# Optimization experiments

Measured on AMD Instinct MI355X. Metric: run time of the kernel, lower is better.

## Reference

```python
import jax, jax.numpy as jnp
import numpy as np

HIDDEN = 512
HEADS = 8
HEAD_DIM = HIDDEN // HEADS
MAX_DIST = 10
B, N = 16, 512
EPS = 1e-5


def _layer_norm(x, g, b):
    mu = jnp.mean(x, axis=-1, keepdims=True)
    var = jnp.mean(jnp.square(x - mu), axis=-1, keepdims=True)
    return (x - mu) * jax.lax.rsqrt(var + EPS) * g + b


def setup_inputs() -> dict:
    key = jax.random.key(0)
    ks = jax.random.split(key, 16)
    s = 0.02
    inp = {
        "x": jax.random.normal(ks[0], (B, N, HIDDEN), jnp.float32),
        "distances": jax.random.randint(ks[1], (B, N, N), 0, MAX_DIST, jnp.int32),
        "edge_features": jax.random.normal(ks[2], (B, N, N), jnp.float32),
        "attn_mask": jax.random.randint(ks[3], (B, N), 0, 2).astype(bool),
        "Wq": jax.random.normal(ks[4], (HIDDEN, HIDDEN), jnp.float32) * s,
        "bq": jnp.zeros((HIDDEN,), jnp.float32),
        "Wk": jax.random.normal(ks[5], (HIDDEN, HIDDEN), jnp.float32) * s,
        "bk": jnp.zeros((HIDDEN,), jnp.float32),
        "Wv": jax.random.normal(ks[6], (HIDDEN, HIDDEN), jnp.float32) * s,
        "bv": jnp.zeros((HIDDEN,), jnp.float32),
        "Wo": jax.random.normal(ks[7], (HIDDEN, HIDDEN), jnp.float32) * s,
        "bo": jnp.zeros((HIDDEN,), jnp.float32),
        "spatial_emb": jax.random.normal(ks[8], (MAX_DIST, HEADS), jnp.float32) * s,
        "edge_w": jax.random.normal(ks[9], (HEADS,), jnp.float32) * s,
        "edge_b": jnp.zeros((HEADS,), jnp.float32),
        "ln1_g": jnp.ones((HIDDEN,), jnp.float32),
        "ln1_b": jnp.zeros((HIDDEN,), jnp.float32),
        "ln2_g": jnp.ones((HIDDEN,), jnp.float32),
        "ln2_b": jnp.zeros((HIDDEN,), jnp.float32),
        "W1": jax.random.normal(ks[10], (HIDDEN, 4 * HIDDEN), jnp.float32) * s,
        "b1": jnp.zeros((4 * HIDDEN,), jnp.float32),
        "W2": jax.random.normal(ks[11], (4 * HIDDEN, HIDDEN), jnp.float32) * s,
        "b2": jnp.zeros((HIDDEN,), jnp.float32),
    }
    return inp


def reference(x, distances, edge_features, attn_mask, Wq, bq, Wk, bk, Wv, bv,
              Wo, bo, spatial_emb, edge_w, edge_b, ln1_g, ln1_b, ln2_g, ln2_b,
              W1, b1, W2, b2):
    b, n, _ = x.shape
    q = (x @ Wq + bq).reshape(b, n, HEADS, HEAD_DIM)
    k = (x @ Wk + bk).reshape(b, n, HEADS, HEAD_DIM)
    v = (x @ Wv + bv).reshape(b, n, HEADS, HEAD_DIM)
    # [b, h, i, j] attention scores
    scores = jnp.einsum('bihd,bjhd->bhij', q, k) / np.sqrt(HEAD_DIM).astype(np.float32)
    spatial_bias = spatial_emb[distances]                       # [b, i, j, h]
    edge_bias = edge_features[..., None] * edge_w + edge_b      # [b, i, j, h]
    scores = scores + jnp.transpose(spatial_bias + edge_bias, (0, 3, 1, 2))
    scores = jnp.where(attn_mask[:, None, None, :], -jnp.inf, scores)
    attn = jax.nn.softmax(scores, axis=-1)
    out = jnp.einsum('bhij,bjhd->bihd', attn, v).reshape(b, n, HIDDEN)
    out = out @ Wo + bo
    h = _layer_norm(x + out, ln1_g, ln1_b)
    ffn = jax.nn.relu(h @ W1 + b1) @ W2 + b2
    return _layer_norm(h + ffn, ln2_g, ln2_b)
```

## Files before the change

kernel.cpp:

```cpp
#include <hip/hip_runtime.h>
#include <stdint.h>
#include <stddef.h>

#define SEQ   512
#define HID   512
#define NHEAD 8
#define HD    64
#define NBATCH 16
#define NTOK  8192
#define MAXD  10
#define LOG2E 1.4426950408889634f

typedef __attribute__((ext_vector_type(8))) short short8;
typedef __attribute__((ext_vector_type(4))) float f32x4;

typedef __attribute__((address_space(3))) void        as3_void;
typedef const __attribute__((address_space(1))) void  as1_cvoid;

#define MFMA16(a,b,c) __builtin_amdgcn_mfma_f32_16x16x32_bf16((a),(b),(c),0,0,0)

__device__ __forceinline__ float bf2f(uint16_t u){ return __uint_as_float(((uint32_t)u)<<16); }
__device__ __forceinline__ uint16_t f2bf(float f){
  uint32_t i = __float_as_uint(f);
  return (uint16_t)((i + 0x7fffu + ((i>>16)&1u)) >> 16);
}
__device__ __forceinline__ uint16_t f2bf_rtz(float f){
  return (uint16_t)(__float_as_uint(f) >> 16);
}

enum { EPI_BF16=0, EPI_F32=3, EPI_RELU=4 };

__global__ __launch_bounds__(256) void prep_kernel(
    const float* __restrict__ x, uint16_t* __restrict__ xb,
    const float* __restrict__ Wq, const float* __restrict__ Wk,
    const float* __restrict__ Wv, const float* __restrict__ Wo,
    const float* __restrict__ W1, const float* __restrict__ W2,
    uint16_t* __restrict__ tq, uint16_t* __restrict__ tk,
    uint16_t* __restrict__ tv, uint16_t* __restrict__ to_,
    uint16_t* __restrict__ t1, uint16_t* __restrict__ t2)
{
  int id = blockIdx.x;
  if (id >= 3072){
    int i = (id-3072)*256 + threadIdx.x;
    if (i < NTOK*HID/4){
      float4 v = *(const float4*)(x + (size_t)i*4);
      *(ushort4*)(xb + (size_t)i*4) =
          make_ushort4(f2bf(v.x), f2bf(v.y), f2bf(v.z), f2bf(v.w));
    }
    return;
  }
  __shared__ uint16_t tile[32][33];
  const float* in; uint16_t* out; int R, C, tx, ty;
  if (id < 1024) {
    int m = id >> 8, loc = id & 255;
    in  = (m==0)?Wq:(m==1)?Wk:(m==2)?Wv:Wo;
    out = (m==0)?tq:(m==1)?tk:(m==2)?tv:to_;
    R = 512; C = 512; ty = loc>>4; tx = loc&15;
  } else if (id < 2048) {
    int loc = id-1024; in=W1; out=t1; R=512; C=2048; ty=loc>>6; tx=loc&63;
  } else {
    int loc = id-2048; in=W2; out=t2; R=2048; C=512; ty=loc>>4; tx=loc&15;
  }
  int bx = tx*32, by = ty*32;
  int lx = threadIdx.x & 31, ly = threadIdx.x >> 5;
  #pragma unroll
  for (int i=ly; i<32; i+=8) tile[i][lx] = f2bf(in[(size_t)(by+i)*C + bx+lx]);
  __syncthreads();
  #pragma unroll
  for (int i=ly; i<32; i+=8) out[(size_t)(bx+i)*R + by+lx] = tile[lx][i];
}

__global__ __launch_bounds__(512) void pack_bias(
    const int*   __restrict__ dist,
    const float* __restrict__ edge,
    const int*   __restrict__ mask,
    uint32_t*    __restrict__ outp)
{
  __shared__ int   dl[16][260];
  __shared__ float el[16][260];
  __shared__ int   ml[512];
  const int b  = blockIdx.y;
  const int it = blockIdx.x;
  const int t  = threadIdx.x;
  ml[t] = mask[b*SEQ + t];

  #pragma unroll
  for (int jh=0; jh<2; ++jh){
    if (jh) __syncthreads();
    {
      const int r  = t >> 5;
      const int c0 = (t & 31) * 8;
      const size_t g = ((size_t)b*SEQ + it*16 + r)*SEQ + jh*256 + c0;
      *(int4*)&dl[r][c0]     = *(const int4*)&dist[g];
      *(int4*)&dl[r][c0+4]   = *(const int4*)&dist[g+4];
      *(float4*)&el[r][c0]   = *(const float4*)&edge[g];
      *(float4*)&el[r][c0+4] = *(const float4*)&edge[g+4];
    }
    __syncthreads();
    {
      const int i   = t & 15;
      const int j0p = (t >> 4) * 8;
      const int jt  = jh*4 + (j0p >> 6);
      const int jn  = (j0p >> 4) & 3;
      const int lg  = (j0p & 15) >> 2;
      uint32_t w[8];
      #pragma unroll
      for (int e=0; e<8; ++e){
        const int jl = j0p + e;
        const int jg = jh*256 + jl;
        const uint32_t d  = (uint32_t)dl[i][jl] & 0xFFu;
        const uint32_t mk = (ml[jg] ? 1u : 0u) << 8;
        w[e] = ((uint32_t)f2bf(el[i][jl]) << 16) | mk | d;
      }
      uint32_t* ob = outp + ((((size_t)b*32 + it)*8 + jt)*64)*16;
      const int lane0 = lg*16 + i, lane1 = (lg+1)*16 + i;
      *(uint4*)&ob[lane0*16 + jn*4] = make_uint4(w[0],w[1],w[2],w[3]);
      *(uint4*)&ob[lane1*16 + jn*4] = make_uint4(w[4],w[5],w[6],w[7]);
    }
  }
}

template<int BM, int BN>
__device__ __forceinline__ void gemm_tile_mainloop(
    const uint16_t* __restrict__ A, const uint16_t* __restrict__ Bt,
    int K, int m0, int n0, uint16_t* lA, uint16_t* lB,
    f32x4 acc[4][(BM==128)?4:((BN==128)?2:1)])
{
  constexpr int NJ  = (BM==128)?4:((BN==128)?2:1);
  constexpr int ARD = BM/32;
  constexpr int BRD = BN/32;
  const int t = threadIdx.x;
  const int w = t>>6, l = t&63;
  const int lg = l>>4, lc = l&15;
  const int wr = (BM==128)?(w>>1):0;
  const int wc = (BM==128)?(w&1):w;
  const int swz = lc & 7;
  const int kSteps = K>>6;

  auto stage = [&](int kt, int buf){
    const int k0 = kt<<6;
    #pragma unroll
    for (int rd=0; rd<ARD; ++rd){
      const int e   = rd*2048 + t*8;
      const int row = e>>6;
      const int col = (((e>>3)&7) ^ (row&7))*8;
      const uint16_t* ga = A + (size_t)(m0+row)*K + (k0+col);
      char* la = (char*)(lA + buf*(BM*64)) + rd*4096 + w*1024;
      __builtin_amdgcn_global_load_lds((as1_cvoid*)ga, (as3_void*)la, 16, 0, 0);
    }
    #pragma unroll
    for (int rd=0; rd<BRD; ++rd){
      const int e   = rd*2048 + t*8;
      const int row = e>>6;
      const int col = (((e>>3)&7) ^ (row&7))*8;
      const uint16_t* gb = Bt + (size_t)(n0+row)*K + (k0+col);
      char* lb = (char*)(lB + buf*(BN*64)) + rd*4096 + w*1024;
      __builtin_amdgcn_global_load_lds((as1_cvoid*)gb, (as3_void*)lb, 16, 0, 0);
    }
  };

  auto compute = [&](const uint16_t* rA, const uint16_t* rB){
    #pragma unroll
    for (int kk=0; kk<2; ++kk){
      const int cc = (kk*4 + lg) ^ swz;
      short8 af[4], bfr[NJ];
      #pragma unroll
      for (int i=0;i<4;i++)
        af[i]  = *(const short8*)&rA[(wr*64 + i*16 + lc)*64 + cc*8];
      #pragma unroll
      for (int j=0;j<NJ;j++)
        bfr[j] = *(const short8*)&rB[(wc*16*NJ + j*16 + lc)*64 + cc*8];
      #pragma unroll
      for (int i=0;i<4;i++)
        #pragma unroll
        for (int j=0;j<NJ;j++)
          acc[i][j] = MFMA16(af[i], bfr[j], acc[i][j]);
    }
  };

  stage(0, 0);
  __syncthreads();
  int cur = 0;
  for (int kt=0; kt<kSteps; ++kt){
    if (kt+1 < kSteps) stage(kt+1, cur^1);
    compute(lA + cur*(BM*64), lB + cur*(BN*64));
    __syncthreads();
    cur ^= 1;
  }
}

template<int EPI, int BM, int BN>
__global__ __launch_bounds__(256,2) void gemm_bt(
    const uint16_t* __restrict__ A, const uint16_t* __restrict__ Bt,
    const float* __restrict__ bias, void* __restrict__ outp,
    int M, int N, int K)
{
  constexpr int NJ = (BM==128)?4:((BN==128)?2:1);
  __shared__ uint16_t lA[2*BM*64];
  __shared__ uint16_t lB[2*BN*64];
  f32x4 acc[4][NJ];
  #pragma unroll
  for (int i=0;i<4;i++)
    #pragma unroll
    for (int j=0;j<NJ;j++){ f32x4 z = {0.f,0.f,0.f,0.f}; acc[i][j]=z; }
  const int m0 = blockIdx.x*BM, n0 = blockIdx.y*BN;
  gemm_tile_mainloop<BM,BN>(A, Bt, K, m0, n0, lA, lB, acc);

  const int t=threadIdx.x, w=t>>6, l=t&63, lg=l>>4, lc=l&15;
  const int wr=(BM==128)?(w>>1):0, wc=(BM==128)?(w&1):w;
  #pragma unroll
  for (int j=0;j<NJ;j++){
    const int col = n0 + wc*16*NJ + j*16 + lc;
    const float bs = bias[col];
    #pragma unroll
    for (int i=0;i<4;i++){
      const int rowb = m0 + wr*64 + i*16 + lg*4;
      #pragma unroll
      for (int r=0;r<4;r++){
        float v = acc[i][j][r] + bs;
        if constexpr (EPI==EPI_RELU)   v = fmaxf(v, 0.f);
        if constexpr (EPI==EPI_F32)
          ((float*)outp)[(size_t)(rowb+r)*N + col] = v;
        else
          ((uint16_t*)outp)[(size_t)(rowb+r)*N + col] = f2bf(v);
      }
    }
  }
}

__global__ __launch_bounds__(256,2) void qkv_gemm(
    const uint16_t* __restrict__ x,
    const uint16_t* __restrict__ wtq, const uint16_t* __restrict__ wtk,
    const uint16_t* __restrict__ wtv,
    const float* __restrict__ bq, const float* __restrict__ bk,
    const float* __restrict__ bv,
    uint16_t* __restrict__ qo, uint16_t* __restrict__ kp,
    uint16_t* __restrict__ vp)
{
  __shared__ uint16_t lA[2*128*64];
  __shared__ uint16_t lB[2*128*64];
  const int z = blockIdx.z;
  const uint16_t* Bt = (z==0)?wtq:(z==1)?wtk:wtv;
  const float*  bias = (z==0)?bq :(z==1)?bk :bv;
  f32x4 acc[4][4];
  #pragma unroll
  for (int i=0;i<4;i++)
    #pragma unroll
    for (int j=0;j<4;j++){ f32x4 zz = {0.f,0.f,0.f,0.f}; acc[i][j]=zz; }
  const int m0 = blockIdx.x*128, n0 = blockIdx.y*128;
  gemm_tile_mainloop<128,128>(x, Bt, HID, m0, n0, lA, lB, acc);

  const int t=threadIdx.x, w=t>>6, l=t&63, lg=l>>4, lc=l&15, wr=w>>1, wc=w&1;
  if (z==0){
    const float scale = 0.125f * LOG2E;
    #pragma unroll
    for (int j=0;j<4;j++){
      const int col = n0 + wc*64 + j*16 + lc;
      const float bs = bias[col];
      #pragma unroll
      for (int i=0;i<4;i++){
        const int rowb = m0 + wr*64 + i*16 + lg*4;
        #pragma unroll
        for (int r=0;r<4;r++)
          qo[(size_t)(rowb+r)*HID + col] = f2bf((acc[i][j][r] + bs)*scale);
      }
    }
  } else if (z==1){
    #pragma unroll
    for (int j=0;j<4;j++){
      const int col = n0 + wc*64 + j*16 + lc;
      const float bs = bias[col];
      const int h_ = col>>6, cm = col&63, kk = cm>>5, lgk = (cm>>3)&3, e = col&7;
      #pragma unroll
      for (int i=0;i<4;i++){
        const int rowb = m0 + wr*64 + i*16 + lg*4;
        #pragma unroll
        for (int r=0;r<4;r++){
          const int tok = rowb + r;
          const int b_ = tok>>9, tl = tok&511;
          const int jt = tl>>6, jn = (tl>>4)&3, lck = tl&15;
          kp[((((size_t)(b_*8+h_)*8 + jt)*4 + jn)*2 + kk)*512
             + (lgk*16 + lck)*8 + e] = f2bf(acc[i][j][r] + bs);
        }
      }
    }
  } else {
    #pragma unroll
    for (int j=0;j<4;j++){
      const int col = n0 + wc*64 + j*16 + lc;
      const float bs = bias[col];
      const int h_ = col>>6, dn = (col>>4)&3, lcv = col&15;
      #pragma unroll
      for (int i=0;i<4;i++){
        const int rowb = m0 + wr*64 + i*16 + lg*4;
        const int b_ = rowb>>9, tl = rowb&511;
        const int jt = tl>>6, kk = (tl>>5)&1, lgv = (tl>>3)&3, e0 = tl&7;
        *(ushort4*)&vp[((((size_t)(b_*8+h_)*8 + jt)*2 + kk)*4 + dn)*512
                       + (lgv*16 + lcv)*8 + e0] =
            make_ushort4(f2bf(acc[i][j][0]+bs), f2bf(acc[i][j][1]+bs),
                         f2bf(acc[i][j][2]+bs), f2bf(acc[i][j][3]+bs));
      }
    }
  }
}

__global__ __launch_bounds__(512,4) void attn_kernel(
    const uint16_t* __restrict__ q,
    const uint16_t* __restrict__ kp,
    const uint16_t* __restrict__ vp,
    const uint32_t* __restrict__ biasp,
    const float*    __restrict__ semb,
    const float*    __restrict__ ew,
    const float*    __restrict__ eb,
    uint16_t* __restrict__ out)
{
  __shared__ float sp_rep[NHEAD][64][11];
  __shared__ uint16_t plds[NHEAD][2][16*64];
  const int b  = blockIdx.y;
  const int it = blockIdx.x;
  const int i0 = it*16;
  const int t  = threadIdx.x;
  const int h  = t>>6, l = t&63, lg = l>>4, lc = l&15;
  for (int i = t; i < NHEAD*64*MAXD; i += 512){
    const int hh = i / (64*MAXD), rem = i % (64*MAXD);
    const int a = rem / MAXD, d = rem % MAXD;
    sp_rep[hh][a][d] = (semb[d*NHEAD + hh] + eb[hh]) * LOG2E;
  }
  __syncthreads();
  const float ewf = ew[h] * LOG2E;
  const float* spl = &sp_rep[h][l][0];
  char* pbase = (char*)&plds[h][0][0];
  const int swz = (lc&7)<<4;

  short8 qf[2];
  #pragma unroll
  for (int kk=0;kk<2;kk++)
    qf[kk] = *(const short8*)&q[(size_t)(b*SEQ + i0 + lc)*HID + h*HD + kk*32 + lg*8];

  const uint4* bp = (const uint4*)(biasp + (((size_t)b*32 + it)*8)*64*16);
  const uint16_t* kpb = kp + (size_t)(b*8+h)*8*4*2*512 + l*8;
  const uint16_t* vpb = vp + (size_t)(b*8+h)*8*2*4*512 + l*8;

  float mrun[2] = {-1e30f, -1e30f};
  float lrun[2] = {0.f, 0.f};
  f32x4 oacc[2][4];
  #pragma unroll
  for (int s=0;s<2;s++)
    #pragma unroll
    for (int dn=0;dn<4;dn++){ f32x4 z={0.f,0.f,0.f,0.f}; oacc[s][dn]=z; }

  #pragma unroll
  for (int p=0; p<4; ++p){
    #pragma unroll
    for (int s=0; s<2; ++s){
      const int jt = s*4 + p;
      uint32_t uw[16];
      {
        const uint4* bq_ = bp + (jt*64 + l)*4;
        *(uint4*)&uw[0]  = bq_[0];
        *(uint4*)&uw[4]  = bq_[1];
        *(uint4*)&uw[8]  = bq_[2];
        *(uint4*)&uw[12] = bq_[3];
      }
      f32x4 st[4];
      #pragma unroll
      for (int jn=0;jn<4;jn++){ f32x4 z={0.f,0.f,0.f,0.f}; st[jn]=z; }
      __builtin_amdgcn_s_setprio(1);
      #pragma unroll
      for (int jn=0;jn<4;jn++){
        #pragma unroll
        for (int kk=0;kk<2;kk++){
          short8 kf = *(const short8*)&kpb[(size_t)((jt*4 + jn)*2 + kk)*512];
          st[jn] = MFMA16(kf, qf[kk], st[jn]);
        }
      }
      __builtin_amdgcn_s_setprio(0);
      float tmax = -1e30f;
      #pragma unroll
      for (int jn=0;jn<4;jn++){
        #pragma unroll
        for (int r=0;r<4;r++){
          const uint32_t u = uw[jn*4+r];
          float sv = st[jn][r] + spl[u & 0xFFu]
                   + bf2f((uint16_t)(u >> 16))*ewf;
          if (u & 0x100u) sv = -1e30f;
          st[jn][r] = sv;
          tmax = fmaxf(tmax, sv);
        }
      }
      {
        float tm = fmaxf(tmax, __shfl_xor(tmax, 16, 64));
        tm = fmaxf(tm, __shfl_xor(tm, 32, 64));
        float mnew = fmaxf(mrun[s], tm);
        mnew = fmaxf(mnew, -1e20f);
        const float c = __builtin_amdgcn_exp2f(mrun[s] - mnew);
        mrun[s] = mnew;
        float lsum = 0.f;
        char* pb = pbase + s*(16*64*2) + lc*128;
        #pragma unroll
        for (int jn=0;jn<4;jn++){
          float p0 = __builtin_amdgcn_exp2f(st[jn][0]-mnew);
          float p1 = __builtin_amdgcn_exp2f(st[jn][1]-mnew);
          float p2 = __builtin_amdgcn_exp2f(st[jn][2]-mnew);
          float p3 = __builtin_amdgcn_exp2f(st[jn][3]-mnew);
          lsum += (p0+p1)+(p2+p3);
          *(ushort4*)(pb + (((jn*16 + lg*4)*2) ^ swz)) =
              make_ushort4(f2bf_rtz(p0), f2bf_rtz(p1),
                           f2bf_rtz(p2), f2bf_rtz(p3));
        }
        lrun[s] = lrun[s]*c + lsum;
        #pragma unroll
        for (int r=0;r<4;r++){
          const float cr = __shfl(c, lg*4+r, 64);
          #pragma unroll
          for (int dn=0;dn<4;dn++) oacc[s][dn][r] *= cr;
        }
      }
    }
    #pragma unroll
    for (int s=0; s<2; ++s){
      const int jt = s*4 + p;
      char* pb = pbase + s*(16*64*2) + lc*128;
      __builtin_amdgcn_s_setprio(1);
      #pragma unroll
      for (int kk=0;kk<2;kk++){
        short8 pa = *(const short8*)(pb + (((kk*32 + lg*8)*2) ^ swz));
        #pragma unroll
        for (int dn=0;dn<4;dn++){
          short8 vb = *(const short8*)&vpb[(size_t)((jt*2 + kk)*4 + dn)*512];
          oacc[s][dn] = MFMA16(pa, vb, oacc[s][dn]);
        }
      }
      __builtin_amdgcn_s_setprio(0);
    }
  }
  {
    const float mm = fmaxf(mrun[0], mrun[1]);
    const float c0 = __builtin_amdgcn_exp2f(mrun[0]-mm);
    const float c1 = __builtin_amdgcn_exp2f(mrun[1]-mm);
    float ls = lrun[0]*c0 + lrun[1]*c1;
    ls += __shfl_xor(ls, 16, 64);
    ls += __shfl_xor(ls, 32, 64);
    const float inv = 1.f/ls;
    #pragma unroll
    for (int r=0;r<4;r++){
      const float cr0 = __shfl(c0, lg*4+r, 64);
      const float cr1 = __shfl(c1, lg*4+r, 64);
      const float ir  = __shfl(inv, lg*4+r, 64);
      const size_t orow = ((size_t)b*SEQ + i0 + lg*4 + r)*HID;
      #pragma unroll
      for (int dn=0;dn<4;dn++)
        out[orow + h*HD + dn*16 + lc] =
            f2bf((oacc[0][dn][r]*cr0 + oacc[1][dn][r]*cr1)*ir);
    }
  }
}

__global__ __launch_bounds__(256) void ln_kernel(
    const uint16_t* __restrict__ a, const float* __restrict__ bsrc,
    const float* __restrict__ g, const float* __restrict__ bb,
    float* __restrict__ of, uint16_t* __restrict__ ob)
{
  const int row = blockIdx.x*4 + (threadIdx.x>>6);
  const int l = threadIdx.x & 63;
  const int c0 = l*8;
  const uint16_t* ar = a    + (size_t)row*HID + c0;
  const float*    br = bsrc + (size_t)row*HID + c0;
  short8 av = *(const short8*)ar;
  float4 b0 = *(const float4*)br;
  float4 b1 = *(const float4*)(br+4);
  float u[8];
  u[0]=bf2f((uint16_t)av[0])+b0.x; u[1]=bf2f((uint16_t)av[1])+b0.y;
  u[2]=bf2f((uint16_t)av[2])+b0.z; u[3]=bf2f((uint16_t)av[3])+b0.w;
  u[4]=bf2f((uint16_t)av[4])+b1.x; u[5]=bf2f((uint16_t)av[5])+b1.y;
  u[6]=bf2f((uint16_t)av[6])+b1.z; u[7]=bf2f((uint16_t)av[7])+b1.w;
  float s=0.f, ss=0.f;
  #pragma unroll
  for (int e=0;e<8;e++){ s += u[e]; ss += u[e]*u[e]; }
  #pragma unroll
  for (int off=32; off>=1; off>>=1){
    s  += __shfl_xor(s,  off, 64);
    ss += __shfl_xor(ss, off, 64);
  }
  const float mu  = s*(1.f/512.f);
  const float inv = rsqrtf(ss*(1.f/512.f) - mu*mu + 1e-5f);
  float4 g0 = *(const float4*)(g + c0),  g1 = *(const float4*)(g + c0 + 4);
  float4 q0 = *(const float4*)(bb + c0), q1 = *(const float4*)(bb + c0 + 4);
  float y[8];
  y[0]=(u[0]-mu)*inv*g0.x+q0.x; y[1]=(u[1]-mu)*inv*g0.y+q0.y;
  y[2]=(u[2]-mu)*inv*g0.z+q0.z; y[3]=(u[3]-mu)*inv*g0.w+q0.w;
  y[4]=(u[4]-mu)*inv*g1.x+q1.x; y[5]=(u[5]-mu)*inv*g1.y+q1.y;
  y[6]=(u[6]-mu)*inv*g1.z+q1.z; y[7]=(u[7]-mu)*inv*g1.w+q1.w;
  if (of){
    float* orow = of + (size_t)row*HID + c0;
    *(float4*)orow     = make_float4(y[0],y[1],y[2],y[3]);
    *(float4*)(orow+4) = make_float4(y[4],y[5],y[6],y[7]);
  }
  if (ob){
    uint16_t* brow = ob + (size_t)row*HID + c0;
    *(ushort4*)brow     = make_ushort4(f2bf(y[0]),f2bf(y[1]),f2bf(y[2]),f2bf(y[3]));
    *(ushort4*)(brow+4) = make_ushort4(f2bf(y[4]),f2bf(y[5]),f2bf(y[6]),f2bf(y[7]));
  }
}

extern "C" void kernel_launch(void* const* d_in, const int* in_sizes, int n_in,
                              void* d_out, int out_size, void* d_ws, size_t ws_size,
                              hipStream_t stream)
{
  (void)in_sizes; (void)n_in; (void)out_size; (void)ws_size;
  const float* x    = (const float*)d_in[0];
  const int*   dist = (const int*)  d_in[1];
  const float* edge = (const float*)d_in[2];
  const int*   mask = (const int*)  d_in[3];
  const float* Wq = (const float*)d_in[4];
  const float* bq = (const float*)d_in[5];
  const float* Wk = (const float*)d_in[6];
  const float* bk = (const float*)d_in[7];
  const float* Wv = (const float*)d_in[8];
  const float* bv = (const float*)d_in[9];
  const float* Wo = (const float*)d_in[10];
  const float* bo = (const float*)d_in[11];
  const float* semb = (const float*)d_in[12];
  const float* ew   = (const float*)d_in[13];
  const float* eb   = (const float*)d_in[14];
  const float* ln1g = (const float*)d_in[15];
  const float* ln1b = (const float*)d_in[16];
  const float* ln2g = (const float*)d_in[17];
  const float* ln2b = (const float*)d_in[18];
  const float* W1 = (const float*)d_in[19];
  const float* b1 = (const float*)d_in[20];
  const float* W2 = (const float*)d_in[21];
  const float* b2 = (const float*)d_in[22];

  char* ws = (char*)d_ws;
  uint16_t* xb16  = (uint16_t*)ws;
  uint16_t* qbuf  = xb16  + (size_t)NTOK*HID;
  uint16_t* kpbuf = qbuf  + (size_t)NTOK*HID;
  uint16_t* vpbuf = kpbuf + (size_t)NTOK*HID;
  uint16_t* aobuf = vpbuf + (size_t)NTOK*HID;
  uint16_t* f1buf = qbuf;
  uint32_t* biasp = (uint32_t*)(ws + (size_t)5*NTOK*HID*2);
  uint16_t* tb16  = (uint16_t*)biasp;
  uint16_t* t2b16 = tb16;
  float*    hbuf  = (float*)((char*)biasp + (size_t)NTOK*HID*4);
  uint16_t* hb16  = (uint16_t*)(hbuf + (size_t)NTOK*HID);
  uint16_t* wt    = hb16 + (size_t)NTOK*HID;
  uint16_t* wtq = wt;
  uint16_t* wtk = wtq + 512*512;
  uint16_t* wtv = wtk + 512*512;
  uint16_t* wto = wtv + 512*512;
  uint16_t* wt1 = wto + 512*512;
  uint16_t* wt2 = wt1 + 512*2048;

  pack_bias<<<dim3(32,16), 512, 0, stream>>>(dist, edge, mask, biasp);

  prep_kernel<<<7168, 256, 0, stream>>>(x, xb16, Wq,Wk,Wv,Wo,W1,W2,
                                        wtq,wtk,wtv,wto,wt1,wt2);

  qkv_gemm<<<dim3(64,4,3), 256, 0, stream>>>(xb16, wtq,wtk,wtv, bq,bk,bv,
                                             qbuf, kpbuf, vpbuf);

  attn_kernel<<<dim3(32,16), 512, 0, stream>>>(qbuf, kpbuf, vpbuf, biasp,
                                               semb, ew, eb, aobuf);

  gemm_bt<EPI_BF16,64,64><<<dim3(128,8), 256, 0, stream>>>(aobuf, wto, bo, tb16, NTOK, HID, HID);

  ln_kernel<<<2048, 256, 0, stream>>>(tb16, x, ln1g, ln1b, hbuf, hb16);

  gemm_bt<EPI_RELU,128,128><<<dim3(64,16), 256, 0, stream>>>(hb16, wt1, b1, f1buf, NTOK, 2048, HID);

  gemm_bt<EPI_BF16,64,64><<<dim3(128,8), 256, 0, stream>>>(f1buf, wt2, b2, t2b16, NTOK, HID, 2048);

  ln_kernel<<<2048, 256, 0, stream>>>(t2b16, hbuf, ln2g, ln2b, (float*)d_out, nullptr);
}
```

Baseline: 159.3 us.

## Fuse bias packing into attention kernel with double-buffered async LDS staging

```diff
diff --git a/kernel.cpp b/kernel.cpp
--- a/kernel.cpp
+++ b/kernel.cpp
@@ -70,56 +70,6 @@
   for (int i=ly; i<32; i+=8) out[(size_t)(bx+i)*R + by+lx] = tile[lx][i];
 }
 
-__global__ __launch_bounds__(512) void pack_bias(
-    const int*   __restrict__ dist,
-    const float* __restrict__ edge,
-    const int*   __restrict__ mask,
-    uint32_t*    __restrict__ outp)
-{
-  __shared__ int   dl[16][260];
-  __shared__ float el[16][260];
-  __shared__ int   ml[512];
-  const int b  = blockIdx.y;
-  const int it = blockIdx.x;
-  const int t  = threadIdx.x;
-  ml[t] = mask[b*SEQ + t];
-
-  #pragma unroll
-  for (int jh=0; jh<2; ++jh){
-    if (jh) __syncthreads();
-    {
-      const int r  = t >> 5;
-      const int c0 = (t & 31) * 8;
-      const size_t g = ((size_t)b*SEQ + it*16 + r)*SEQ + jh*256 + c0;
-      *(int4*)&dl[r][c0]     = *(const int4*)&dist[g];
-      *(int4*)&dl[r][c0+4]   = *(const int4*)&dist[g+4];
-      *(float4*)&el[r][c0]   = *(const float4*)&edge[g];
-      *(float4*)&el[r][c0+4] = *(const float4*)&edge[g+4];
-    }
-    __syncthreads();
-    {
-      const int i   = t & 15;
-      const int j0p = (t >> 4) * 8;
-      const int jt  = jh*4 + (j0p >> 6);
-      const int jn  = (j0p >> 4) & 3;
-      const int lg  = (j0p & 15) >> 2;
-      uint32_t w[8];
-      #pragma unroll
-      for (int e=0; e<8; ++e){
-        const int jl = j0p + e;
-        const int jg = jh*256 + jl;
-        const uint32_t d  = (uint32_t)dl[i][jl] & 0xFFu;
-        const uint32_t mk = (ml[jg] ? 1u : 0u) << 8;
-        w[e] = ((uint32_t)f2bf(el[i][jl]) << 16) | mk | d;
-      }
-      uint32_t* ob = outp + ((((size_t)b*32 + it)*8 + jt)*64)*16;
-      const int lane0 = lg*16 + i, lane1 = (lg+1)*16 + i;
-      *(uint4*)&ob[lane0*16 + jn*4] = make_uint4(w[0],w[1],w[2],w[3]);
-      *(uint4*)&ob[lane1*16 + jn*4] = make_uint4(w[4],w[5],w[6],w[7]);
-    }
-  }
-}
-
 template<int BM, int BN>
 __device__ __forceinline__ void gemm_tile_mainloop(
     const uint16_t* __restrict__ A, const uint16_t* __restrict__ Bt,
@@ -308,27 +258,52 @@
     const uint16_t* __restrict__ q,
     const uint16_t* __restrict__ kp,
     const uint16_t* __restrict__ vp,
-    const uint32_t* __restrict__ biasp,
+    const int*      __restrict__ dist,
+    const float*    __restrict__ edge,
+    const int*      __restrict__ mask,
     const float*    __restrict__ semb,
     const float*    __restrict__ ew,
     const float*    __restrict__ eb,
     uint16_t* __restrict__ out)
 {
-  __shared__ float sp_rep[NHEAD][64][11];
+  __shared__ float sp_rep[NHEAD][32][11];
   __shared__ uint16_t plds[NHEAD][2][16*64];
+  __shared__ int   dstage[2][16][64];
+  __shared__ float estage[2][16][64];
+  __shared__ float mlf[512];
   const int b  = blockIdx.y;
   const int it = blockIdx.x;
   const int i0 = it*16;
   const int t  = threadIdx.x;
   const int h  = t>>6, l = t&63, lg = l>>4, lc = l&15;
-  for (int i = t; i < NHEAD*64*MAXD; i += 512){
-    const int hh = i / (64*MAXD), rem = i % (64*MAXD);
+  for (int i = t; i < NHEAD*32*MAXD; i += 512){
+    const int hh = i / (32*MAXD), rem = i % (32*MAXD);
     const int a = rem / MAXD, d = rem % MAXD;
     sp_rep[hh][a][d] = (semb[d*NHEAD + hh] + eb[hh]) * LOG2E;
   }
-  __syncthreads();
+  mlf[t] = mask[b*SEQ + t] ? -1e30f : 0.f;
+
+  auto stage_bias = [&](int jt, int buf){
+    const int srow = l>>4, schk = l&15;
+    if (h < 4){
+      const int row = h*4 + srow;
+      const int sc  = schk ^ (row&7);
+      const int* src = dist + ((size_t)b*SEQ + i0 + row)*SEQ + jt*64 + sc*4;
+      char* dst = (char*)&dstage[buf][0][0] + h*1024;
+      __builtin_amdgcn_global_load_lds((as1_cvoid*)src, (as3_void*)dst, 16, 0, 0);
+    } else {
+      const int row = (h-4)*4 + srow;
+      const int sc  = schk ^ (row&7);
+      const float* src = edge + ((size_t)b*SEQ + i0 + row)*SEQ + jt*64 + sc*4;
+      char* dst = (char*)&estage[buf][0][0] + (h-4)*1024;
+      __builtin_amdgcn_global_load_lds((as1_cvoid*)src, (as3_void*)dst, 16, 0, 0);
+    }
+  };
+
+  stage_bias(0, 0);
+
   const float ewf = ew[h] * LOG2E;
-  const float* spl = &sp_rep[h][l][0];
+  const float* spl = &sp_rep[h][l&31][0];
   char* pbase = (char*)&plds[h][0][0];
   const int swz = (lc&7)<<4;
 
@@ -337,7 +312,6 @@
   for (int kk=0;kk<2;kk++)
     qf[kk] = *(const short8*)&q[(size_t)(b*SEQ + i0 + lc)*HID + h*HD + kk*32 + lg*8];
 
-  const uint4* bp = (const uint4*)(biasp + (((size_t)b*32 + it)*8)*64*16);
   const uint16_t* kpb = kp + (size_t)(b*8+h)*8*4*2*512 + l*8;
   const uint16_t* vpb = vp + (size_t)(b*8+h)*8*2*4*512 + l*8;
 
@@ -349,77 +323,82 @@
     #pragma unroll
     for (int dn=0;dn<4;dn++){ f32x4 z={0.f,0.f,0.f,0.f}; oacc[s][dn]=z; }
 
-  #pragma unroll
-  for (int p=0; p<4; ++p){
-    #pragma unroll
-    for (int s=0; s<2; ++s){
-      const int jt = s*4 + p;
-      uint32_t uw[16];
-      {
-        const uint4* bq_ = bp + (jt*64 + l)*4;
-        *(uint4*)&uw[0]  = bq_[0];
-        *(uint4*)&uw[4]  = bq_[1];
-        *(uint4*)&uw[8]  = bq_[2];
-        *(uint4*)&uw[12] = bq_[3];
-      }
-      f32x4 st[4];
-      #pragma unroll
-      for (int jn=0;jn<4;jn++){ f32x4 z={0.f,0.f,0.f,0.f}; st[jn]=z; }
-      __builtin_amdgcn_s_setprio(1);
+  __syncthreads();
+
+  int cur = 0;
+  #pragma unroll
+  for (int step=0; step<8; ++step){
+    const int s  = step & 1;
+    const int p  = step >> 1;
+    const int jt = s*4 + p;
+    if (step < 7){
+      const int nstep = step+1;
+      stage_bias(((nstep&1)*4) + (nstep>>1), cur^1);
+    }
+    f32x4 st[4];
+    #pragma unroll
+    for (int jn=0;jn<4;jn++){ f32x4 z={0.f,0.f,0.f,0.f}; st[jn]=z; }
+    __builtin_amdgcn_s_setprio(1);
+    #pragma unroll
+    for (int jn=0;jn<4;jn++){
+      #pragma unroll
+      for (int kk=0;kk<2;kk++){
+        short8 kf = *(const short8*)&kpb[(size_t)((jt*4 + jn)*2 + kk)*512];
+        st[jn] = MFMA16(kf, qf[kk], st[jn]);
+      }
+    }
+    __builtin_amdgcn_s_setprio(0);
+    float tmax = -1e30f;
+    {
+      const char* db  = (const char*)&dstage[cur][0][0] + lc*256;
+      const char* ebp = (const char*)&estage[cur][0][0] + lc*256;
+      const float* mrow = &mlf[jt*64];
       #pragma unroll
       for (int jn=0;jn<4;jn++){
-        #pragma unroll
-        for (int kk=0;kk<2;kk++){
-          short8 kf = *(const short8*)&kpb[(size_t)((jt*4 + jn)*2 + kk)*512];
-          st[jn] = MFMA16(kf, qf[kk], st[jn]);
-        }
-      }
-      __builtin_amdgcn_s_setprio(0);
-      float tmax = -1e30f;
-      #pragma unroll
-      for (int jn=0;jn<4;jn++){
+        const int off = (((jn*4+lg) ^ (lc&7))*16);
+        int4   d4 = *(const int4*)  (db  + off);
+        float4 e4 = *(const float4*)(ebp + off);
+        float4 m4 = *(const float4*)&mrow[jn*16 + lg*4];
+        const int   da[4] = {d4.x, d4.y, d4.z, d4.w};
+        const float ea[4] = {e4.x, e4.y, e4.z, e4.w};
+        const float ma[4] = {m4.x, m4.y, m4.z, m4.w};
         #pragma unroll
         for (int r=0;r<4;r++){
-          const uint32_t u = uw[jn*4+r];
-          float sv = st[jn][r] + spl[u & 0xFFu]
-                   + bf2f((uint16_t)(u >> 16))*ewf;
-          if (u & 0x100u) sv = -1e30f;
+          float sv = st[jn][r] + spl[da[r]] + ea[r]*ewf + ma[r];
           st[jn][r] = sv;
           tmax = fmaxf(tmax, sv);
         }
       }
-      {
-        float tm = fmaxf(tmax, __shfl_xor(tmax, 16, 64));
-        tm = fmaxf(tm, __shfl_xor(tm, 32, 64));
-        float mnew = fmaxf(mrun[s], tm);
-        mnew = fmaxf(mnew, -1e20f);
-        const float c = __builtin_amdgcn_exp2f(mrun[s] - mnew);
-        mrun[s] = mnew;
-        float lsum = 0.f;
-        char* pb = pbase + s*(16*64*2) + lc*128;
+    }
+    {
+      float tm = fmaxf(tmax, __shfl_xor(tmax, 16, 64));
+      tm = fmaxf(tm, __shfl_xor(tm, 32, 64));
+      float mnew = fmaxf(mrun[s], tm);
+      mnew = fmaxf(mnew, -1e20f);
+      const float c = __builtin_amdgcn_exp2f(mrun[s] - mnew);
+      mrun[s] = mnew;
+      float lsum = 0.f;
+      char* pb = pbase + s*(16*64*2) + lc*128;
+      #pragma unroll
+      for (int jn=0;jn<4;jn++){
+        float p0 = __builtin_amdgcn_exp2f(st[jn][0]-mnew);
+        float p1 = __builtin_amdgcn_exp2f(st[jn][1]-mnew);
+        float p2 = __builtin_amdgcn_exp2f(st[jn][2]-mnew);
+        float p3 = __builtin_amdgcn_exp2f(st[jn][3]-mnew);
+        lsum += (p0+p1)+(p2+p3);
+        *(ushort4*)(pb + (((jn*16 + lg*4)*2) ^ swz)) =
+            make_ushort4(f2bf_rtz(p0), f2bf_rtz(p1),
+                         f2bf_rtz(p2), f2bf_rtz(p3));
+      }
+      lrun[s] = lrun[s]*c + lsum;
+      #pragma unroll
+      for (int r=0;r<4;r++){
+        const float cr = __shfl(c, lg*4+r, 64);
         #pragma unroll
-        for (int jn=0;jn<4;jn++){
-          float p0 = __builtin_amdgcn_exp2f(st[jn][0]-mnew);
-          float p1 = __builtin_amdgcn_exp2f(st[jn][1]-mnew);
-          float p2 = __builtin_amdgcn_exp2f(st[jn][2]-mnew);
-          float p3 = __builtin_amdgcn_exp2f(st[jn][3]-mnew);
-          lsum += (p0+p1)+(p2+p3);
-          *(ushort4*)(pb + (((jn*16 + lg*4)*2) ^ swz)) =
-              make_ushort4(f2bf_rtz(p0), f2bf_rtz(p1),
-                           f2bf_rtz(p2), f2bf_rtz(p3));
-        }
-        lrun[s] = lrun[s]*c + lsum;
-        #pragma unroll
-        for (int r=0;r<4;r++){
-          const float cr = __shfl(c, lg*4+r, 64);
-          #pragma unroll
-          for (int dn=0;dn<4;dn++) oacc[s][dn][r] *= cr;
-        }
-      }
-    }
-    #pragma unroll
-    for (int s=0; s<2; ++s){
-      const int jt = s*4 + p;
+        for (int dn=0;dn<4;dn++) oacc[s][dn][r] *= cr;
+      }
+    }
+    {
       char* pb = pbase + s*(16*64*2) + lc*128;
       __builtin_amdgcn_s_setprio(1);
       #pragma unroll
@@ -433,6 +412,8 @@
       }
       __builtin_amdgcn_s_setprio(0);
     }
+    __syncthreads();
+    cur ^= 1;
   }
   {
     const float mm = fmaxf(mrun[0], mrun[1]);
@@ -539,10 +520,9 @@
   uint16_t* vpbuf = kpbuf + (size_t)NTOK*HID;
   uint16_t* aobuf = vpbuf + (size_t)NTOK*HID;
   uint16_t* f1buf = qbuf;
-  uint32_t* biasp = (uint32_t*)(ws + (size_t)5*NTOK*HID*2);
-  uint16_t* tb16  = (uint16_t*)biasp;
+  uint16_t* tb16  = (uint16_t*)(ws + (size_t)5*NTOK*HID*2);
   uint16_t* t2b16 = tb16;
-  float*    hbuf  = (float*)((char*)biasp + (size_t)NTOK*HID*4);
+  float*    hbuf  = (float*)((char*)tb16 + (size_t)NTOK*HID*4);
   uint16_t* hb16  = (uint16_t*)(hbuf + (size_t)NTOK*HID);
   uint16_t* wt    = hb16 + (size_t)NTOK*HID;
   uint16_t* wtq = wt;
@@ -552,15 +532,14 @@
   uint16_t* wt1 = wto + 512*512;
   uint16_t* wt2 = wt1 + 512*2048;
 
-  pack_bias<<<dim3(32,16), 512, 0, stream>>>(dist, edge, mask, biasp);
-
   prep_kernel<<<7168, 256, 0, stream>>>(x, xb16, Wq,Wk,Wv,Wo,W1,W2,
                                         wtq,wtk,wtv,wto,wt1,wt2);
 
   qkv_gemm<<<dim3(64,4,3), 256, 0, stream>>>(xb16, wtq,wtk,wtv, bq,bk,bv,
                                              qbuf, kpbuf, vpbuf);
 
-  attn_kernel<<<dim3(32,16), 512, 0, stream>>>(qbuf, kpbuf, vpbuf, biasp,
+  attn_kernel<<<dim3(32,16), 512, 0, stream>>>(qbuf, kpbuf, vpbuf,
+                                               dist, edge, mask,
                                                semb, ew, eb, aobuf);
 
   gemm_bt<EPI_BF16,64,64><<<dim3(128,8), 256, 0, stream>>>(aobuf, wto, bo, tb16, NTOK, HID, HID);
```

Result: slower. 180.7 us (+13.4%).

## Fuse bias packing into QKV GEMM launch via interleaved block roles

Applied to the files above, without the earlier changes.

```diff
diff --git a/kernel.cpp b/kernel.cpp
--- a/kernel.cpp
+++ b/kernel.cpp
@@ -70,56 +70,6 @@
   for (int i=ly; i<32; i+=8) out[(size_t)(bx+i)*R + by+lx] = tile[lx][i];
 }
 
-__global__ __launch_bounds__(512) void pack_bias(
-    const int*   __restrict__ dist,
-    const float* __restrict__ edge,
-    const int*   __restrict__ mask,
-    uint32_t*    __restrict__ outp)
-{
-  __shared__ int   dl[16][260];
-  __shared__ float el[16][260];
-  __shared__ int   ml[512];
-  const int b  = blockIdx.y;
-  const int it = blockIdx.x;
-  const int t  = threadIdx.x;
-  ml[t] = mask[b*SEQ + t];
-
-  #pragma unroll
-  for (int jh=0; jh<2; ++jh){
-    if (jh) __syncthreads();
-    {
-      const int r  = t >> 5;
-      const int c0 = (t & 31) * 8;
-      const size_t g = ((size_t)b*SEQ + it*16 + r)*SEQ + jh*256 + c0;
-      *(int4*)&dl[r][c0]     = *(const int4*)&dist[g];
-      *(int4*)&dl[r][c0+4]   = *(const int4*)&dist[g+4];
-      *(float4*)&el[r][c0]   = *(const float4*)&edge[g];
-      *(float4*)&el[r][c0+4] = *(const float4*)&edge[g+4];
-    }
-    __syncthreads();
-    {
-      const int i   = t & 15;
-      const int j0p = (t >> 4) * 8;
-      const int jt  = jh*4 + (j0p >> 6);
-      const int jn  = (j0p >> 4) & 3;
-      const int lg  = (j0p & 15) >> 2;
-      uint32_t w[8];
-      #pragma unroll
-      for (int e=0; e<8; ++e){
-        const int jl = j0p + e;
-        const int jg = jh*256 + jl;
-        const uint32_t d  = (uint32_t)dl[i][jl] & 0xFFu;
-        const uint32_t mk = (ml[jg] ? 1u : 0u) << 8;
-        w[e] = ((uint32_t)f2bf(el[i][jl]) << 16) | mk | d;
-      }
-      uint32_t* ob = outp + ((((size_t)b*32 + it)*8 + jt)*64)*16;
-      const int lane0 = lg*16 + i, lane1 = (lg+1)*16 + i;
-      *(uint4*)&ob[lane0*16 + jn*4] = make_uint4(w[0],w[1],w[2],w[3]);
-      *(uint4*)&ob[lane1*16 + jn*4] = make_uint4(w[4],w[5],w[6],w[7]);
-    }
-  }
-}
-
 template<int BM, int BN>
 __device__ __forceinline__ void gemm_tile_mainloop(
     const uint16_t* __restrict__ A, const uint16_t* __restrict__ Bt,
@@ -228,18 +178,86 @@
   }
 }
 
-__global__ __launch_bounds__(256,2) void qkv_gemm(
+__global__ __launch_bounds__(256,2) void qkv_pack(
     const uint16_t* __restrict__ x,
     const uint16_t* __restrict__ wtq, const uint16_t* __restrict__ wtk,
     const uint16_t* __restrict__ wtv,
     const float* __restrict__ bq, const float* __restrict__ bk,
     const float* __restrict__ bv,
     uint16_t* __restrict__ qo, uint16_t* __restrict__ kp,
-    uint16_t* __restrict__ vp)
-{
-  __shared__ uint16_t lA[2*128*64];
-  __shared__ uint16_t lB[2*128*64];
-  const int z = blockIdx.z;
+    uint16_t* __restrict__ vp,
+    const int*   __restrict__ dist,
+    const float* __restrict__ edge,
+    const int*   __restrict__ mask,
+    uint32_t*    __restrict__ biasp)
+{
+  __shared__ char smem[2*2*128*64*2];
+  const int t = threadIdx.x;
+  const int flat = blockIdx.x + 64*(blockIdx.y + 4*blockIdx.z);
+
+  if ((flat & 3) == 3){
+    int*   dl = (int*)smem;
+    float* el = (float*)(smem + 16*260*4);
+    int*   ml = (int*)(smem + 2*16*260*4);
+    #define DL(r,c) dl[(r)*260+(c)]
+    #define EL(r,c) el[(r)*260+(c)]
+    #pragma unroll
+    for (int u0=0; u0<2; ++u0){
+      const int u  = (flat>>2)*2 + u0;
+      const int b  = u>>5, it = u&31;
+      __syncthreads();
+      ml[t]     = mask[b*SEQ + t];
+      ml[t+256] = mask[b*SEQ + t + 256];
+      #pragma unroll
+      for (int jh=0; jh<2; ++jh){
+        if (jh) __syncthreads();
+        {
+          const int r  = t >> 4;
+          const int c0 = (t & 15) * 16;
+          const size_t g = ((size_t)b*SEQ + it*16 + r)*SEQ + jh*256 + c0;
+          *(int4*)&DL(r,c0)      = *(const int4*)&dist[g];
+          *(int4*)&DL(r,c0+4)    = *(const int4*)&dist[g+4];
+          *(int4*)&DL(r,c0+8)    = *(const int4*)&dist[g+8];
+          *(int4*)&DL(r,c0+12)   = *(const int4*)&dist[g+12];
+          *(float4*)&EL(r,c0)    = *(const float4*)&edge[g];
+          *(float4*)&EL(r,c0+4)  = *(const float4*)&edge[g+4];
+          *(float4*)&EL(r,c0+8)  = *(const float4*)&edge[g+8];
+          *(float4*)&EL(r,c0+12) = *(const float4*)&edge[g+12];
+        }
+        __syncthreads();
+        {
+          const int i   = t & 15;
+          const int j0p = (t >> 4) * 16;
+          const int jn  = (j0p >> 4) & 3;
+          const int jt  = jh*4 + (j0p >> 6);
+          uint32_t wv[16];
+          #pragma unroll
+          for (int e=0; e<16; ++e){
+            const int jl = j0p + e;
+            const int jg = jh*256 + jl;
+            const uint32_t d  = (uint32_t)DL(i,jl) & 0xFFu;
+            const uint32_t mk = (ml[jg] ? 1u : 0u) << 8;
+            wv[e] = ((uint32_t)f2bf(EL(i,jl)) << 16) | mk | d;
+          }
+          uint32_t* ob = biasp + ((((size_t)b*32 + it)*8 + jt)*64)*16;
+          #pragma unroll
+          for (int lgq=0; lgq<4; ++lgq)
+            *(uint4*)&ob[(lgq*16 + i)*16 + jn*4] =
+                make_uint4(wv[lgq*4], wv[lgq*4+1], wv[lgq*4+2], wv[lgq*4+3]);
+        }
+      }
+    }
+    #undef DL
+    #undef EL
+    return;
+  }
+
+  const int g  = (flat>>2)*3 + (flat&3);
+  const int m0 = (g & 63) * 128;
+  const int n0 = ((g >> 6) & 3) * 128;
+  const int z  = g >> 8;
+  uint16_t* lA = (uint16_t*)smem;
+  uint16_t* lB = lA + 2*128*64;
   const uint16_t* Bt = (z==0)?wtq:(z==1)?wtk:wtv;
   const float*  bias = (z==0)?bq :(z==1)?bk :bv;
   f32x4 acc[4][4];
@@ -247,10 +265,9 @@
   for (int i=0;i<4;i++)
     #pragma unroll
     for (int j=0;j<4;j++){ f32x4 zz = {0.f,0.f,0.f,0.f}; acc[i][j]=zz; }
-  const int m0 = blockIdx.x*128, n0 = blockIdx.y*128;
   gemm_tile_mainloop<128,128>(x, Bt, HID, m0, n0, lA, lB, acc);
 
-  const int t=threadIdx.x, w=t>>6, l=t&63, lg=l>>4, lc=l&15, wr=w>>1, wc=w&1;
+  const int w=t>>6, l=t&63, lg=l>>4, lc=l&15, wr=w>>1, wc=w&1;
   if (z==0){
     const float scale = 0.125f * LOG2E;
     #pragma unroll
@@ -552,13 +569,12 @@
   uint16_t* wt1 = wto + 512*512;
   uint16_t* wt2 = wt1 + 512*2048;
 
-  pack_bias<<<dim3(32,16), 512, 0, stream>>>(dist, edge, mask, biasp);
-
   prep_kernel<<<7168, 256, 0, stream>>>(x, xb16, Wq,Wk,Wv,Wo,W1,W2,
                                         wtq,wtk,wtv,wto,wt1,wt2);
 
-  qkv_gemm<<<dim3(64,4,3), 256, 0, stream>>>(xb16, wtq,wtk,wtv, bq,bk,bv,
-                                             qbuf, kpbuf, vpbuf);
+  qkv_pack<<<dim3(64,4,4), 256, 0, stream>>>(xb16, wtq,wtk,wtv, bq,bk,bv,
+                                             qbuf, kpbuf, vpbuf,
+                                             dist, edge, mask, biasp);
 
   attn_kernel<<<dim3(32,16), 512, 0, stream>>>(qbuf, kpbuf, vpbuf, biasp,
                                                semb, ew, eb, aobuf);
```

Measured after the change: 155.3 us. 1.03x faster.
